# Kernel tuning notes

Hardware: AMD Instinct MI355X
Metric: run time of the kernel (lower is better)

Reference implementation:

```python
import jax, jax.numpy as jnp
import numpy as np

B, T, E, H, Dh = 1, 2048, 1024, 16, 64
ROPE_BASE = 10000.0
NUM_BLOCK = 12  # transformer depth, only used for fc_2 init scale


def setup_inputs() -> dict:
    key = jax.random.key(0)
    k1, k2, k3 = jax.random.split(key, 3)
    x = jax.random.normal(k1, (B, T, E), dtype=jnp.float32)
    W1 = jax.random.normal(k2, (3 * E, E), dtype=jnp.float32) * 0.02
    W2 = jax.random.normal(k3, (E, E), dtype=jnp.float32) * (0.02 / np.sqrt(2.0 * NUM_BLOCK))
    return {"x": x, "W1": W1, "W2": W2}


def _rope(t):
    # t: (B, T, H, Dh). Rotate-half RoPE with base 10000.
    half = Dh // 2
    inv_freq = 1.0 / (ROPE_BASE ** (jnp.arange(0, half, dtype=jnp.float32) / half))
    ang = jnp.arange(T, dtype=jnp.float32)[:, None] * inv_freq[None, :]  # (T, half)
    cos = jnp.cos(ang)[None, :, None, :]
    sin = jnp.sin(ang)[None, :, None, :]
    t1, t2 = t[..., :half], t[..., half:]
    return jnp.concatenate([t1 * cos - t2 * sin, t2 * cos + t1 * sin], axis=-1)


def reference(x, W1, W2):
    # fused QKV projection
    qkv = x @ W1.T                                   # (B, T, 3E)
    q, k, v = jnp.split(qkv, 3, axis=-1)
    q = q.reshape(B, T, H, Dh)
    k = k.reshape(B, T, H, Dh)
    v = v.reshape(B, T, H, Dh)
    q = _rope(q)
    k = _rope(k)
    # causal attention (block-sparse flex-attention == per-sample causal mask)
    scale = 1.0 / np.sqrt(Dh)
    scores = jnp.einsum('bthd,bshd->bhts', q, k) * scale   # (B, H, T, T)
    causal = jnp.tril(jnp.ones((T, T), dtype=bool))
    scores = jnp.where(causal[None, None], scores, jnp.finfo(scores.dtype).min)
    p = jax.nn.softmax(scores, axis=-1)
    o = jnp.einsum('bhts,bshd->bthd', p, v).reshape(B, T, E)
    return o @ W2.T
```

## Files before the change

kernel.cpp:

```cpp
#include <hip/hip_runtime.h>
#include <math.h>

#define TT 2048
#define EE 1024
#define HH 16
#define DH 64

typedef unsigned short u16;
typedef __attribute__((ext_vector_type(8))) short bf16x8;
typedef __attribute__((ext_vector_type(4))) float f32x4;
typedef __attribute__((address_space(1))) unsigned int uint_g;
typedef __attribute__((address_space(3))) unsigned int uint_l;

__device__ __forceinline__ u16 f2bf(float f) {
  unsigned u = __float_as_uint(f);
  u += 0x7fffu + ((u >> 16) & 1u);
  return (u16)(u >> 16);
}

__global__ __launch_bounds__(256) void cvt_all(
    const float* __restrict__ x, const float* __restrict__ W1,
    const float* __restrict__ W2, u16* __restrict__ xb, u16* __restrict__ w1b,
    u16* __restrict__ w2b) {
  int i = blockIdx.x * 256 + threadIdx.x;
  const float* s;
  u16* d;
  if (i < 262144) {
    s = x; d = xb;
  } else if (i < 262144 + 393216) {
    i -= 262144; s = W1; d = w1b;
  } else {
    i -= 262144 + 393216; s = W2; d = w2b;
  }
  const float4* s4 = (const float4*)s;
  float4 a = s4[2 * i], b = s4[2 * i + 1];
  bf16x8 o;
  o[0] = (short)f2bf(a.x); o[1] = (short)f2bf(a.y);
  o[2] = (short)f2bf(a.z); o[3] = (short)f2bf(a.w);
  o[4] = (short)f2bf(b.x); o[5] = (short)f2bf(b.y);
  o[6] = (short)f2bf(b.z); o[7] = (short)f2bf(b.w);
  *(bf16x8*)&d[8 * i] = o;
}

__global__ void rope_table(float* __restrict__ cs, float* __restrict__ sn) {
  int i = blockIdx.x * 256 + threadIdx.x;
  int t = i >> 5;
  int d = i & 31;
  float inv = powf(10000.f, -((float)d) / 32.f);
  float ang = (float)t * inv;
  cs[i] = (float)cos((double)ang);
  sn[i] = (float)sin((double)ang);
}

template <int EPI>
__global__ __launch_bounds__(256) void gemm_mfma(
    const u16* __restrict__ A, const u16* __restrict__ B, float* __restrict__ C,
    u16* __restrict__ q16, u16* __restrict__ k16, u16* __restrict__ vt,
    const float* __restrict__ cs, const float* __restrict__ sn, int M, int N,
    int K) {
  __shared__ u16 smem[8192];
  const int tid = threadIdx.x;
  const int lane = tid & 63;
  const int wid = tid >> 6;
  const int wr = wid >> 1, wc = wid & 1;
  const int m0 = blockIdx.y * 128, n0 = blockIdx.x * 128;

  const u16* gp[4];
  int lo[4];
#pragma unroll
  for (int q = 0; q < 4; q++) {
    int o = (wid * 4 + q) * 1024 + lane * 16;
    lo[q] = o >> 1;
    if (o < 8192) {
      int row = o >> 6, col = (o >> 1) & 31;
      gp[q] = A + (size_t)(m0 + row) * K + col;
    } else {
      int o2 = o - 8192;
      int row = o2 >> 6, col = (o2 >> 1) & 31;
      gp[q] = B + (size_t)(n0 + row) * K + col;
    }
  }

  const int a_off = (wr * 64 + (lane & 15)) * 32 + (lane >> 4) * 8;
  const int b_off = 4096 + (wc * 64 + (lane & 15)) * 32 + (lane >> 4) * 8;

  f32x4 acc[4][4];
#pragma unroll
  for (int i = 0; i < 4; i++)
#pragma unroll
    for (int j = 0; j < 4; j++) acc[i][j] = f32x4{0.f, 0.f, 0.f, 0.f};

  for (int k0 = 0; k0 < K; k0 += 32) {
    __syncthreads();
#pragma unroll
    for (int q = 0; q < 4; q++) {
      __builtin_amdgcn_global_load_lds((const uint_g*)gp[q],
                                       (uint_l*)&smem[lo[q]], 16, 0, 0);
      gp[q] += 32;
    }
    __syncthreads();
    bf16x8 af[4], bg[4];
#pragma unroll
    for (int i = 0; i < 4; i++) af[i] = *(const bf16x8*)&smem[a_off + i * 512];
#pragma unroll
    for (int j = 0; j < 4; j++) bg[j] = *(const bf16x8*)&smem[b_off + j * 512];
#pragma unroll
    for (int i = 0; i < 4; i++)
#pragma unroll
      for (int j = 0; j < 4; j++)
        acc[i][j] = __builtin_amdgcn_mfma_f32_16x16x32_bf16(af[i], bg[j],
                                                            acc[i][j], 0, 0, 0);
  }

  const int rbase = (lane >> 4) * 4;
  const int ncol = lane & 15;
  if (EPI == 0) {
#pragma unroll
    for (int i = 0; i < 4; i++) {
      int m = m0 + wr * 64 + i * 16 + rbase;
#pragma unroll
      for (int j = 0; j < 4; j++) {
        int n = n0 + wc * 64 + j * 16 + ncol;
#pragma unroll
        for (int r = 0; r < 4; r++) C[(size_t)(m + r) * N + n] = acc[i][j][r];
      }
    }
  } else {
    const int which = n0 >> 10;
    if (which == 2) {
#pragma unroll
      for (int j = 0; j < 4; j++) {
        int n = n0 + wc * 64 + j * 16 + ncol;
        int h = (n >> 6) & 15, d = n & 63;
#pragma unroll
        for (int i = 0; i < 4; i++) {
          int m = m0 + wr * 64 + i * 16 + rbase;
#pragma unroll
          for (int r = 0; r < 4; r++)
            vt[((size_t)h * DH + d) * TT + m + r] = f2bf(acc[i][j][r]);
        }
      }
    } else {
      u16* dst = (which == 0) ? q16 : k16;
#pragma unroll
      for (int j = 0; j < 2; j++) {
        int n = n0 + wc * 64 + j * 16 + ncol;
        int h = (n >> 6) & 15, d = n & 63;
#pragma unroll
        for (int i = 0; i < 4; i++) {
          int mrow = m0 + wr * 64 + i * 16 + rbase;
#pragma unroll
          for (int r = 0; r < 4; r++) {
            int t = mrow + r;
            float c = cs[t * 32 + d];
            float s = sn[t * 32 + d];
            float a = acc[i][j][r];
            float b = acc[i][j + 2][r];
            size_t off = ((size_t)h * TT + t) * DH + d;
            dst[off] = f2bf(a * c - b * s);
            dst[off + 32] = f2bf(b * c + a * s);
          }
        }
      }
    }
  }
}

__global__ __launch_bounds__(64) void attn_mfma(
    const u16* __restrict__ Q, const u16* __restrict__ K,
    const u16* __restrict__ Vt, u16* __restrict__ O) {
  __shared__ u16 P_lds[16][72];
  const int lane = threadIdx.x;
  const int l15 = lane & 15;
  const int l4 = lane >> 4;
  const int rbase = l4 * 4;
  const int h = blockIdx.x & 15;
  const int tile = 127 - (blockIdx.x >> 4);
  const int qbase = tile << 4;
  const int nc = ((qbase + 15) >> 6) + 1;

  const u16* Qh = Q + (size_t)h * TT * DH;
  const u16* Kh = K + (size_t)h * TT * DH;
  const u16* Vh = Vt + (size_t)h * DH * TT;

  const int qrow = qbase + l15;
  bf16x8 qf0 = *(const bf16x8*)&Qh[(size_t)qrow * DH + l4 * 8];
  bf16x8 qf1 = *(const bf16x8*)&Qh[(size_t)qrow * DH + 32 + l4 * 8];

  float m[4], l[4];
  f32x4 oacc[4];
#pragma unroll
  for (int r = 0; r < 4; r++) {
    m[r] = -1e30f;
    l[r] = 0.f;
  }
#pragma unroll
  for (int j = 0; j < 4; j++) oacc[j] = f32x4{0.f, 0.f, 0.f, 0.f};

  for (int ch = 0; ch < nc; ch++) {
    const int kbase = ch << 6;
    f32x4 s[4];
#pragma unroll
    for (int j = 0; j < 4; j++) s[j] = f32x4{0.f, 0.f, 0.f, 0.f};
#pragma unroll
    for (int j = 0; j < 4; j++) {
      bf16x8 kf0 =
          *(const bf16x8*)&Kh[(size_t)(kbase + j * 16 + l15) * DH + l4 * 8];
      bf16x8 kf1 = *(const bf16x8*)&Kh[(size_t)(kbase + j * 16 + l15) * DH +
                                       32 + l4 * 8];
      s[j] = __builtin_amdgcn_mfma_f32_16x16x32_bf16(qf0, kf0, s[j], 0, 0, 0);
      s[j] = __builtin_amdgcn_mfma_f32_16x16x32_bf16(qf1, kf1, s[j], 0, 0, 0);
    }
#pragma unroll
    for (int j = 0; j < 4; j++) {
      s[j][0] *= 0.125f; s[j][1] *= 0.125f;
      s[j][2] *= 0.125f; s[j][3] *= 0.125f;
    }
    if (ch == nc - 1) {
#pragma unroll
      for (int j = 0; j < 4; j++) {
        int kg = kbase + j * 16 + l15;
#pragma unroll
        for (int r = 0; r < 4; r++) {
          int qg = qbase + rbase + r;
          if (kg > qg) s[j][r] = -1e30f;
        }
      }
    }
#pragma unroll
    for (int r = 0; r < 4; r++) {
      float rm = fmaxf(fmaxf(s[0][r], s[1][r]), fmaxf(s[2][r], s[3][r]));
      rm = fmaxf(rm, __shfl_xor(rm, 1));
      rm = fmaxf(rm, __shfl_xor(rm, 2));
      rm = fmaxf(rm, __shfl_xor(rm, 4));
      rm = fmaxf(rm, __shfl_xor(rm, 8));
      const float mn = fmaxf(m[r], rm);
      const float corr = __expf(m[r] - mn);
      m[r] = mn;
      float rs = 0.f;
#pragma unroll
      for (int j = 0; j < 4; j++) {
        float p = __expf(s[j][r] - mn);
        s[j][r] = p;
        rs += p;
      }
      rs += __shfl_xor(rs, 1);
      rs += __shfl_xor(rs, 2);
      rs += __shfl_xor(rs, 4);
      rs += __shfl_xor(rs, 8);
      l[r] = l[r] * corr + rs;
      oacc[0][r] *= corr;
      oacc[1][r] *= corr;
      oacc[2][r] *= corr;
      oacc[3][r] *= corr;
    }
#pragma unroll
    for (int j = 0; j < 4; j++)
#pragma unroll
      for (int r = 0; r < 4; r++)
        P_lds[rbase + r][j * 16 + l15] = f2bf(s[j][r]);
#pragma unroll
    for (int ks = 0; ks < 2; ks++) {
      bf16x8 pa = *(const bf16x8*)&P_lds[l15][ks * 32 + l4 * 8];
#pragma unroll
      for (int j = 0; j < 4; j++) {
        bf16x8 vf = *(const bf16x8*)&Vh[(size_t)(j * 16 + l15) * TT + kbase +
                                        ks * 32 + l4 * 8];
        oacc[j] =
            __builtin_amdgcn_mfma_f32_16x16x32_bf16(pa, vf, oacc[j], 0, 0, 0);
      }
    }
  }
#pragma unroll
  for (int r = 0; r < 4; r++) {
    const float inv = 1.f / l[r];
    const int qg = qbase + rbase + r;
#pragma unroll
    for (int j = 0; j < 4; j++)
      O[(size_t)qg * EE + h * DH + j * 16 + l15] = f2bf(oacc[j][r] * inv);
  }
}

extern "C" void kernel_launch(void* const* d_in, const int* in_sizes, int n_in,
                              void* d_out, int out_size, void* d_ws,
                              size_t ws_size, hipStream_t stream) {
  const float* x = (const float*)d_in[0];
  const float* W1 = (const float*)d_in[1];
  const float* W2 = (const float*)d_in[2];
  float* out = (float*)d_out;

  float* ws = (float*)d_ws;
  const size_t HTD = (size_t)HH * TT * DH;
  float* cs = ws;
  float* sn = cs + (size_t)TT * 32;
  u16* qb16 = (u16*)(sn + (size_t)TT * 32);
  u16* kb16 = qb16 + HTD;
  u16* vt16 = kb16 + HTD;
  u16* obb = vt16 + HTD;
  u16* xb = obb + (size_t)TT * EE;
  u16* w1b = xb + (size_t)TT * EE;
  u16* w2b = w1b + (size_t)3 * EE * EE;

  rope_table<<<(TT * 32) / 256, 256, 0, stream>>>(cs, sn);
  cvt_all<<<786432 / 256, 256, 0, stream>>>(x, W1, W2, xb, w1b, w2b);
  gemm_mfma<1><<<dim3(3 * EE / 128, TT / 128), 256, 0, stream>>>(
      xb, w1b, nullptr, qb16, kb16, vt16, cs, sn, TT, 3 * EE, EE);
  attn_mfma<<<2048, 64, 0, stream>>>(qb16, kb16, vt16, obb);
  gemm_mfma<0><<<dim3(EE / 128, TT / 128), 256, 0, stream>>>(
      obb, w2b, out, nullptr, nullptr, nullptr, nullptr, nullptr, TT, EE, EE);
}
```

Before: 201.9 us.

## Split causal attention over KV chunks and merge partials in a combine kernel

The attention kernel now splits each 16-row query tile's causal KV range into slices of at most four 64-key chunks. Each slice is its own workgroup, which writes an unnormalized bf16 partial output plus row max and sum to workspace. A new combine kernel then merges the partials with log-sum-exp rescaling. This evens out the load imbalance of long causal rows and raises parallelism (9216 small blocks instead of 2048), at the cost of an extra launch, extra global traffic for the partials, and bf16 rounding of the unnormalized partials.

Measured after the change: 208.3 us. 3.2% more time.

```diff
diff --git a/kernel.cpp b/kernel.cpp
--- a/kernel.cpp
+++ b/kernel.cpp
@@ -16,6 +16,9 @@
   unsigned u = __float_as_uint(f);
   u += 0x7fffu + ((u >> 16) & 1u);
   return (u16)(u >> 16);
+}
+__device__ __forceinline__ float bf2f(u16 v) {
+  return __uint_as_float(((unsigned)v) << 16);
 }
 
 __global__ __launch_bounds__(256) void cvt_all(
@@ -166,18 +169,32 @@
   }
 }
 
-__global__ __launch_bounds__(64) void attn_mfma(
+__global__ __launch_bounds__(64) void attn_split(
     const u16* __restrict__ Q, const u16* __restrict__ K,
-    const u16* __restrict__ Vt, u16* __restrict__ O) {
+    const u16* __restrict__ Vt, u16* __restrict__ op, float* __restrict__ ml) {
   __shared__ u16 P_lds[16][72];
   const int lane = threadIdx.x;
   const int l15 = lane & 15;
   const int l4 = lane >> 4;
   const int rbase = l4 * 4;
-  const int h = blockIdx.x & 15;
-  const int tile = 127 - (blockIdx.x >> 4);
-  const int qbase = tile << 4;
-  const int nc = ((qbase + 15) >> 6) + 1;
+  const int bid = blockIdx.x;
+  const int h = bid & 15;
+  const int b = bid >> 4;
+  int g = 0;
+#pragma unroll
+  for (int gg = 1; gg < 8; gg++)
+    if (b >= 8 * gg * (gg + 1)) g = gg;
+  const int sp = g + 1;
+  const int idx = b - 8 * g * (g + 1);
+  const int tq = idx / sp;
+  const int t = 16 * g + tq;
+  const int s = idx - tq * sp;
+  const int u = h * 576 + b;
+
+  const int nc = (t >> 2) + 1;
+  const int c0 = s * 4;
+  const int c1 = min(c0 + 4, nc);
+  const int qbase = t << 4;
 
   const u16* Qh = Q + (size_t)h * TT * DH;
   const u16* Kh = K + (size_t)h * TT * DH;
@@ -197,24 +214,26 @@
 #pragma unroll
   for (int j = 0; j < 4; j++) oacc[j] = f32x4{0.f, 0.f, 0.f, 0.f};
 
-  for (int ch = 0; ch < nc; ch++) {
+  for (int ch = c0; ch < c1; ch++) {
     const int kbase = ch << 6;
-    f32x4 s[4];
-#pragma unroll
-    for (int j = 0; j < 4; j++) s[j] = f32x4{0.f, 0.f, 0.f, 0.f};
+    f32x4 s4v[4];
+#pragma unroll
+    for (int j = 0; j < 4; j++) s4v[j] = f32x4{0.f, 0.f, 0.f, 0.f};
 #pragma unroll
     for (int j = 0; j < 4; j++) {
       bf16x8 kf0 =
           *(const bf16x8*)&Kh[(size_t)(kbase + j * 16 + l15) * DH + l4 * 8];
       bf16x8 kf1 = *(const bf16x8*)&Kh[(size_t)(kbase + j * 16 + l15) * DH +
                                        32 + l4 * 8];
-      s[j] = __builtin_amdgcn_mfma_f32_16x16x32_bf16(qf0, kf0, s[j], 0, 0, 0);
-      s[j] = __builtin_amdgcn_mfma_f32_16x16x32_bf16(qf1, kf1, s[j], 0, 0, 0);
+      s4v[j] =
+          __builtin_amdgcn_mfma_f32_16x16x32_bf16(qf0, kf0, s4v[j], 0, 0, 0);
+      s4v[j] =
+          __builtin_amdgcn_mfma_f32_16x16x32_bf16(qf1, kf1, s4v[j], 0, 0, 0);
     }
 #pragma unroll
     for (int j = 0; j < 4; j++) {
-      s[j][0] *= 0.125f; s[j][1] *= 0.125f;
-      s[j][2] *= 0.125f; s[j][3] *= 0.125f;
+      s4v[j][0] *= 0.125f; s4v[j][1] *= 0.125f;
+      s4v[j][2] *= 0.125f; s4v[j][3] *= 0.125f;
     }
     if (ch == nc - 1) {
 #pragma unroll
@@ -223,13 +242,14 @@
 #pragma unroll
         for (int r = 0; r < 4; r++) {
           int qg = qbase + rbase + r;
-          if (kg > qg) s[j][r] = -1e30f;
+          if (kg > qg) s4v[j][r] = -1e30f;
         }
       }
     }
 #pragma unroll
     for (int r = 0; r < 4; r++) {
-      float rm = fmaxf(fmaxf(s[0][r], s[1][r]), fmaxf(s[2][r], s[3][r]));
+      float rm =
+          fmaxf(fmaxf(s4v[0][r], s4v[1][r]), fmaxf(s4v[2][r], s4v[3][r]));
       rm = fmaxf(rm, __shfl_xor(rm, 1));
       rm = fmaxf(rm, __shfl_xor(rm, 2));
       rm = fmaxf(rm, __shfl_xor(rm, 4));
@@ -240,8 +260,8 @@
       float rs = 0.f;
 #pragma unroll
       for (int j = 0; j < 4; j++) {
-        float p = __expf(s[j][r] - mn);
-        s[j][r] = p;
+        float p = __expf(s4v[j][r] - mn);
+        s4v[j][r] = p;
         rs += p;
       }
       rs += __shfl_xor(rs, 1);
@@ -258,7 +278,7 @@
     for (int j = 0; j < 4; j++)
 #pragma unroll
       for (int r = 0; r < 4; r++)
-        P_lds[rbase + r][j * 16 + l15] = f2bf(s[j][r]);
+        P_lds[rbase + r][j * 16 + l15] = f2bf(s4v[j][r]);
 #pragma unroll
     for (int ks = 0; ks < 2; ks++) {
       bf16x8 pa = *(const bf16x8*)&P_lds[l15][ks * 32 + l4 * 8];
@@ -271,14 +291,58 @@
       }
     }
   }
-#pragma unroll
-  for (int r = 0; r < 4; r++) {
-    const float inv = 1.f / l[r];
-    const int qg = qbase + rbase + r;
-#pragma unroll
-    for (int j = 0; j < 4; j++)
-      O[(size_t)qg * EE + h * DH + j * 16 + l15] = f2bf(oacc[j][r] * inv);
-  }
+  if (l15 == 0) {
+#pragma unroll
+    for (int r = 0; r < 4; r++) {
+      ml[(size_t)u * 32 + rbase + r] = m[r];
+      ml[(size_t)u * 32 + 16 + rbase + r] = l[r];
+    }
+  }
+  u16* ou = op + (size_t)u * 1024;
+#pragma unroll
+  for (int j = 0; j < 4; j++)
+#pragma unroll
+    for (int r = 0; r < 4; r++)
+      ou[(rbase + r) * 64 + j * 16 + l15] = f2bf(oacc[j][r]);
+}
+
+__global__ __launch_bounds__(64) void attn_combine(
+    const u16* __restrict__ op, const float* __restrict__ ml,
+    u16* __restrict__ O) {
+  const int lane = threadIdx.x;
+  const int row = lane >> 2;
+  const int c0 = (lane & 3) * 16;
+  const int h = blockIdx.x & 15;
+  const int t = blockIdx.x >> 4;
+  const int g = t >> 4;
+  const int ns = g + 1;
+  const int u0 = h * 576 + 8 * g * (g + 1) + (t - 16 * g) * ns;
+
+  float mg = -1e30f;
+  for (int s = 0; s < ns; s++)
+    mg = fmaxf(mg, ml[(size_t)(u0 + s) * 32 + row]);
+  float acc[16];
+#pragma unroll
+  for (int i = 0; i < 16; i++) acc[i] = 0.f;
+  float lg = 0.f;
+  for (int s = 0; s < ns; s++) {
+    const size_t u = u0 + s;
+    const float w = __expf(ml[u * 32 + row] - mg);
+    lg += w * ml[u * 32 + 16 + row];
+    const u16* po = op + u * 1024 + row * 64 + c0;
+    bf16x8 v0 = *(const bf16x8*)po;
+    bf16x8 v1 = *(const bf16x8*)(po + 8);
+#pragma unroll
+    for (int i = 0; i < 8; i++) {
+      acc[i] += w * bf2f((u16)v0[i]);
+      acc[8 + i] += w * bf2f((u16)v1[i]);
+    }
+  }
+  const float inv = 1.f / lg;
+  const int qg = (t << 4) + row;
+  u16* dst = O + (size_t)qg * EE + h * DH + c0;
+#pragma unroll
+  for (int i = 0; i < 16; i++) dst[i] = f2bf(acc[i] * inv);
 }
 
 extern "C" void kernel_launch(void* const* d_in, const int* in_sizes, int n_in,
@@ -293,19 +357,22 @@
   const size_t HTD = (size_t)HH * TT * DH;
   float* cs = ws;
   float* sn = cs + (size_t)TT * 32;
-  u16* qb16 = (u16*)(sn + (size_t)TT * 32);
+  float* ml = sn + (size_t)TT * 32;
+  u16* qb16 = (u16*)(ml + (size_t)9216 * 32);
   u16* kb16 = qb16 + HTD;
   u16* vt16 = kb16 + HTD;
   u16* obb = vt16 + HTD;
   u16* xb = obb + (size_t)TT * EE;
   u16* w1b = xb + (size_t)TT * EE;
   u16* w2b = w1b + (size_t)3 * EE * EE;
+  u16* op = w2b + (size_t)EE * EE;
 
   rope_table<<<(TT * 32) / 256, 256, 0, stream>>>(cs, sn);
   cvt_all<<<786432 / 256, 256, 0, stream>>>(x, W1, W2, xb, w1b, w2b);
   gemm_mfma<1><<<dim3(3 * EE / 128, TT / 128), 256, 0, stream>>>(
       xb, w1b, nullptr, qb16, kb16, vt16, cs, sn, TT, 3 * EE, EE);
-  attn_mfma<<<2048, 64, 0, stream>>>(qb16, kb16, vt16, obb);
+  attn_split<<<9216, 64, 0, stream>>>(qb16, kb16, vt16, op, ml);
+  attn_combine<<<2048, 64, 0, stream>>>(op, ml, obb);
   gemm_mfma<0><<<dim3(EE / 128, TT / 128), 256, 0, stream>>>(
       obb, w2b, out, nullptr, nullptr, nullptr, nullptr, nullptr, TT, EE, EE);
 }
```
